# Optimization experiments

Hardware: AMD Instinct MI355X
Metric: run time of the kernel (lower is better)

Reference implementation:

```python
import jax, jax.numpy as jnp
import numpy as np

B, TE, TD, HE, HD = 16, 512, 64, 512, 512


def setup_inputs() -> dict:
    key = jax.random.key(0)
    k1, k2, k3, k4, k5 = jax.random.split(key, 5)
    return {
        "encoder_out_seq": jax.random.normal(k1, (B, TE, HE), dtype=jnp.float32),
        "decoder_out_seq": jax.random.normal(k2, (B, TD, HD), dtype=jnp.float32),
        "W_a": jax.random.normal(k3, (HE, HE), dtype=jnp.float32) * 0.05,
        "U_a": jax.random.normal(k4, (HD, HE), dtype=jnp.float32) * 0.05,
        "V_a": jax.random.normal(k5, (HE, 1), dtype=jnp.float32) * 0.05,
    }


def reference(encoder_out_seq, decoder_out_seq, W_a, U_a, V_a):
    # Bahdanau additive attention, batched over all decoder steps at once
    # (the original K.rnn loop over Td is embarrassingly parallel).
    Ws = jnp.einsum('bte,eh->bth', encoder_out_seq, W_a)   # [B,Te,He]
    Uh = jnp.einsum('bdk,kh->bdh', decoder_out_seq, U_a)   # [B,Td,He]
    # additive combine + tanh: [B,Td,Te,He]
    act = jnp.tanh(Ws[:, None, :, :] + Uh[:, :, None, :])
    e = jnp.einsum('bdth,h->bdt', act, V_a[:, 0])          # [B,Td,Te]
    e = jax.nn.softmax(e, axis=-1)                          # attention weights
    c = jnp.einsum('bdt,bth->bdh', e, encoder_out_seq)      # [B,Td,He] context
    return (c, e)
```

## Files before the change

kernel.cpp:

```cpp
#include <hip/hip_runtime.h>
#include <hip/hip_bf16.h>

#define BB 16
#define TE 512
#define TD 64
#define HE 512

#define PRESCALE 2.8853900817779268f

typedef __attribute__((ext_vector_type(8))) short bf16x8;
typedef __attribute__((ext_vector_type(4))) float f32x4;

__device__ __forceinline__ float fexp2(float x) {
#if __has_builtin(__builtin_amdgcn_exp2f)
    return __builtin_amdgcn_exp2f(x);
#else
    return exp2f(x);
#endif
}
__device__ __forceinline__ float frcp(float x) {
#if __has_builtin(__builtin_amdgcn_rcpf)
    return __builtin_amdgcn_rcpf(x);
#else
    return __fdividef(1.f, x);
#endif
}

__device__ __forceinline__ void split2(float x, unsigned short& h, unsigned short& l) {
    __hip_bfloat16 hb = __float2bfloat16(x);
    h = *(unsigned short*)&hb;
    float r = x - __bfloat162float(hb);
    __hip_bfloat16 lb = __float2bfloat16(r);
    l = *(unsigned short*)&lb;
}

__device__ __forceinline__ void gload16(const unsigned short* g, void* l) {
    __builtin_amdgcn_global_load_lds(
        (const __attribute__((address_space(1))) unsigned int*)g,
        (__attribute__((address_space(3))) unsigned int*)l, 16, 0, 0);
}


__device__ __forceinline__ void tile_load(const float* __restrict__ src, int ld,
                                          float (*tile)[64], int tid)
{
#pragma unroll
    for (int p = 0; p < 4; ++p) {
        const int f = p * 256 + tid;
        const int r = f >> 4, c4 = f & 15;
        const float4 v = *(const float4*)&src[(size_t)r * ld + c4 * 4];
        *(float4*)&tile[r][((c4 ^ (r & 7))) << 2] = v;
    }
}

__device__ __forceinline__ void tile_outA(float (*tile)[64],
                                          unsigned short* __restrict__ H,
                                          unsigned short* __restrict__ L,
                                          size_t Ms, size_t sg_base, size_t m_base, int tid)
{
#pragma unroll
    for (int p = 0; p < 2; ++p) {
        const int task = p * 256 + tid;
        const int s = task >> 6, mm = task & 63;
        const float4 x = *(const float4*)&tile[mm][(((s << 1)    ) ^ (mm & 7)) << 2];
        const float4 y = *(const float4*)&tile[mm][(((s << 1) | 1) ^ (mm & 7)) << 2];
        ushort4 ha, la, hb, lb;
        split2(x.x, ha.x, la.x); split2(x.y, ha.y, la.y);
        split2(x.z, ha.z, la.z); split2(x.w, ha.w, la.w);
        split2(y.x, hb.x, lb.x); split2(y.y, hb.y, lb.y);
        split2(y.z, hb.z, lb.z); split2(y.w, hb.w, lb.w);
        const size_t o = ((sg_base + s) * Ms + m_base + mm) * 8;
        *(ushort4*)&H[o] = ha; *(ushort4*)&H[o + 4] = hb;
        *(ushort4*)&L[o] = la; *(ushort4*)&L[o + 4] = lb;
    }
}

__device__ __forceinline__ void tile_outT(float (*tile)[64],
                                          unsigned short* __restrict__ H,
                                          unsigned short* __restrict__ L,
                                          size_t Ns, size_t sg_base, size_t n_base, int tid)
{
#pragma unroll
    for (int p = 0; p < 2; ++p) {
        const int task = p * 256 + tid;
        const int s2 = task >> 6, hh = task & 63;
        float v[8];
#pragma unroll
        for (int q = 0; q < 8; ++q) {
            const int r = s2 * 8 + q;
            v[q] = tile[r][((((hh >> 2)) ^ (r & 7)) << 2) + (hh & 3)];
        }
        ushort4 ha, la, hb, lb;
        split2(v[0], ha.x, la.x); split2(v[1], ha.y, la.y);
        split2(v[2], ha.z, la.z); split2(v[3], ha.w, la.w);
        split2(v[4], hb.x, lb.x); split2(v[5], hb.y, lb.y);
        split2(v[6], hb.z, lb.z); split2(v[7], hb.w, lb.w);
        const size_t o = ((sg_base + s2) * Ns + n_base + hh) * 8;
        *(ushort4*)&H[o] = ha; *(ushort4*)&H[o + 4] = hb;
        *(ushort4*)&L[o] = la; *(ushort4*)&L[o + 4] = lb;
    }
}

__global__ __launch_bounds__(256)
void split_all(const float* __restrict__ enc,
               unsigned short* __restrict__ eAh, unsigned short* __restrict__ eAl,
               unsigned short* __restrict__ eTh, unsigned short* __restrict__ eTl,
               const float* __restrict__ dec,
               unsigned short* __restrict__ dH, unsigned short* __restrict__ dL,
               const float* __restrict__ Wa,
               unsigned short* __restrict__ wH, unsigned short* __restrict__ wL,
               const float* __restrict__ Ua,
               unsigned short* __restrict__ uH, unsigned short* __restrict__ uL)
{
    __shared__ float tile[64][64];
    const int tid = threadIdx.x;
    const int x = blockIdx.x, y = blockIdx.y, z = blockIdx.z;

    if (z < 16) {
        if (y < 8) {
            const int h0 = x * 64, t0 = y * 64;
            const size_t bo = (size_t)z * TE * HE;
            tile_load(enc + bo + (size_t)t0 * HE + h0, HE, tile, tid);
            __syncthreads();
            tile_outA(tile, eAh, eAl, (size_t)BB * TE, h0 >> 3, (size_t)z * TE + t0, tid);
            tile_outT(tile, eTh + bo, eTl + bo, HE, t0 >> 3, h0, tid);
        } else if (y == 8) {
            const int m0 = z * 64, h0 = x * 64;
            tile_load(dec + (size_t)m0 * HE + h0, HE, tile, tid);
            __syncthreads();
            tile_outA(tile, dH, dL, (size_t)BB * TD, h0 >> 3, m0, tid);
        }
        return;
    }
    const int yy = (y < 8) ? y : y - 8;
    const float* X = (y < 8) ? Wa : Ua;
    unsigned short* H = (y < 8) ? wH : uH;
    unsigned short* L = (y < 8) ? wL : uL;
    const int r0 = yy * 64, c0 = x * 64;
    tile_load(X + (size_t)r0 * HE + c0, HE, tile, tid);
    __syncthreads();
    tile_outT(tile, H, L, HE, r0 >> 3, c0, tid);
}

__global__ __launch_bounds__(256)
void gemm_ws_uh(const unsigned short* __restrict__ eAh, const unsigned short* __restrict__ eAl,
                const unsigned short* __restrict__ wBh, const unsigned short* __restrict__ wBl,
                float* __restrict__ Ew,
                const unsigned short* __restrict__ dAh, const unsigned short* __restrict__ dAl,
                const unsigned short* __restrict__ uBh, const unsigned short* __restrict__ uBl,
                float* __restrict__ Eu)
{
    __shared__ char smem[2][32768];

    const int tid  = threadIdx.x;
    const int lane = tid & 63;
    const int wave = tid >> 6;
    const int wr = wave >> 1, wc = wave & 1;
    const int fr = lane & 15, fg = lane >> 4;

    const int hw = blockIdx.y * 4 + blockIdx.x;
    const int f  = (hw & 7) * 36 + (hw >> 3);
    const int bx = f & 3, by = f >> 2;

    const unsigned short *Ahi, *Alo, *Bhi, *Blo;
    float* C;
    int M, row0;
    if (by < 64) {
        Ahi = eAh; Alo = eAl; Bhi = wBh; Blo = wBl; C = Ew;
        M = BB * TE; row0 = by * 128;
    } else {
        Ahi = dAh; Alo = dAl; Bhi = uBh; Blo = uBl; C = Eu;
        M = BB * TD; row0 = (by - 64) * 128;
    }
    const int N = HE, K = HE;
    const int col0 = bx * 128;

    f32x4 acc[4][4];
#pragma unroll
    for (int mi = 0; mi < 4; ++mi)
#pragma unroll
        for (int ni = 0; ni < 4; ++ni)
            acc[mi][ni] = (f32x4){0.f, 0.f, 0.f, 0.f};

    auto STAGE = [&](int buf, int k0) {
#pragma unroll
        for (int c = 0; c < 2; ++c) {
            const int bi  = (c * 4 + wave) * 64 + lane;
            const int g   = bi >> 7;
            const int idx = bi & 127;
            int mrow = row0 + idx; if (mrow >= M) mrow -= M;
            const int ncol = col0 + idx;
            const size_t ao = ((size_t)((k0 >> 3) + g) * M + mrow) * 8;
            const size_t bo = ((size_t)((k0 >> 3) + g) * N + ncol) * 8;
            const int lb = (c * 4 + wave) * 1024;
            gload16(Ahi + ao, smem[buf] + lb);
            gload16(Alo + ao, smem[buf] + 8192 + lb);
            gload16(Bhi + bo, smem[buf] + 16384 + lb);
            gload16(Blo + bo, smem[buf] + 24576 + lb);
        }
    };

    STAGE(0, 0);

    int buf = 0;
    for (int k0 = 0; k0 < K; k0 += 32) {
        if (k0 + 32 < K) {
            STAGE(buf ^ 1, k0 + 32);
            asm volatile("s_waitcnt vmcnt(8)\n\ts_barrier" ::: "memory");
        } else {
            asm volatile("s_waitcnt vmcnt(0)\n\ts_barrier" ::: "memory");
        }

        const int gb = fg << 7;
        bf16x8 ah[4], al[4], bh[4], bl[4];
#pragma unroll
        for (int mi = 0; mi < 4; ++mi) {
            const int off = (gb + wr * 64 + mi * 16 + fr) * 16;
            ah[mi] = *(const bf16x8*)(smem[buf] + off);
            al[mi] = *(const bf16x8*)(smem[buf] + 8192 + off);
        }
#pragma unroll
        for (int ni = 0; ni < 4; ++ni) {
            const int off = (gb + wc * 64 + ni * 16 + fr) * 16;
            bh[ni] = *(const bf16x8*)(smem[buf] + 16384 + off);
            bl[ni] = *(const bf16x8*)(smem[buf] + 24576 + off);
        }
#pragma unroll
        for (int mi = 0; mi < 4; ++mi)
#pragma unroll
            for (int ni = 0; ni < 4; ++ni) {
                acc[mi][ni] = __builtin_amdgcn_mfma_f32_16x16x32_bf16(ah[mi], bh[ni], acc[mi][ni], 0, 0, 0);
                acc[mi][ni] = __builtin_amdgcn_mfma_f32_16x16x32_bf16(ah[mi], bl[ni], acc[mi][ni], 0, 0, 0);
                acc[mi][ni] = __builtin_amdgcn_mfma_f32_16x16x32_bf16(al[mi], bh[ni], acc[mi][ni], 0, 0, 0);
            }
        asm volatile("s_barrier" ::: "memory");
        buf ^= 1;
    }

#pragma unroll
    for (int mi = 0; mi < 4; ++mi) {
        const int rbase = row0 + wr * 64 + mi * 16 + fg * 4;
#pragma unroll
        for (int ni = 0; ni < 4; ++ni) {
            const int col = col0 + wc * 64 + ni * 16 + fr;
#pragma unroll
            for (int r = 0; r < 4; ++r) {
                const int row = rbase + r;
                if (row < M) C[(size_t)row * N + col] = fexp2(acc[mi][ni][r] * PRESCALE);
            }
        }
    }
}

__global__ __launch_bounds__(256)
void gemm_mfma3(const unsigned short* __restrict__ Ahi, const unsigned short* __restrict__ Alo,
                const unsigned short* __restrict__ Bhi, const unsigned short* __restrict__ Blo,
                float* __restrict__ C, int M, int N, int K,
                long long sA, long long sB, long long sC)
{
    __shared__ char smem[2][32768];

    const int tid  = threadIdx.x;
    const int lane = tid & 63;
    const int wave = tid >> 6;
    const int wr = wave >> 1, wc = wave & 1;
    const int fr = lane & 15, fg = lane >> 4;
    const int row0 = blockIdx.y * 128;
    const int col0 = blockIdx.x * 128;

    Ahi += (size_t)blockIdx.z * sA; Alo += (size_t)blockIdx.z * sA;
    Bhi += (size_t)blockIdx.z * sB; Blo += (size_t)blockIdx.z * sB;
    C   += (size_t)blockIdx.z * sC;

    f32x4 acc[4][4];
#pragma unroll
    for (int mi = 0; mi < 4; ++mi)
#pragma unroll
        for (int ni = 0; ni < 4; ++ni)
            acc[mi][ni] = (f32x4){0.f, 0.f, 0.f, 0.f};

    auto STAGE = [&](int buf, int k0) {
#pragma unroll
        for (int c = 0; c < 2; ++c) {
            const int bi  = (c * 4 + wave) * 64 + lane;
            const int g   = bi >> 7;
            const int idx = bi & 127;
            int mrow = row0 + idx; if (mrow >= M) mrow -= M;
            const int ncol = col0 + idx;
            const size_t ao = ((size_t)((k0 >> 3) + g) * M + mrow) * 8;
            const size_t bo = ((size_t)((k0 >> 3) + g) * N + ncol) * 8;
            const int lb = (c * 4 + wave) * 1024;
            gload16(Ahi + ao, smem[buf] + lb);
            gload16(Alo + ao, smem[buf] + 8192 + lb);
            gload16(Bhi + bo, smem[buf] + 16384 + lb);
            gload16(Blo + bo, smem[buf] + 24576 + lb);
        }
    };

    STAGE(0, 0);

    int buf = 0;
    for (int k0 = 0; k0 < K; k0 += 32) {
        if (k0 + 32 < K) {
            STAGE(buf ^ 1, k0 + 32);
            asm volatile("s_waitcnt vmcnt(8)\n\ts_barrier" ::: "memory");
        } else {
            asm volatile("s_waitcnt vmcnt(0)\n\ts_barrier" ::: "memory");
        }

        const int gb = fg << 7;
        bf16x8 ah[4], al[4], bh[4], bl[4];
#pragma unroll
        for (int mi = 0; mi < 4; ++mi) {
            const int off = (gb + wr * 64 + mi * 16 + fr) * 16;
            ah[mi] = *(const bf16x8*)(smem[buf] + off);
            al[mi] = *(const bf16x8*)(smem[buf] + 8192 + off);
        }
#pragma unroll
        for (int ni = 0; ni < 4; ++ni) {
            const int off = (gb + wc * 64 + ni * 16 + fr) * 16;
            bh[ni] = *(const bf16x8*)(smem[buf] + 16384 + off);
            bl[ni] = *(const bf16x8*)(smem[buf] + 24576 + off);
        }
#pragma unroll
        for (int mi = 0; mi < 4; ++mi)
#pragma unroll
            for (int ni = 0; ni < 4; ++ni) {
                acc[mi][ni] = __builtin_amdgcn_mfma_f32_16x16x32_bf16(ah[mi], bh[ni], acc[mi][ni], 0, 0, 0);
                acc[mi][ni] = __builtin_amdgcn_mfma_f32_16x16x32_bf16(ah[mi], bl[ni], acc[mi][ni], 0, 0, 0);
                acc[mi][ni] = __builtin_amdgcn_mfma_f32_16x16x32_bf16(al[mi], bh[ni], acc[mi][ni], 0, 0, 0);
            }
        asm volatile("s_barrier" ::: "memory");
        buf ^= 1;
    }

#pragma unroll
    for (int mi = 0; mi < 4; ++mi) {
        const int rbase = row0 + wr * 64 + mi * 16 + fg * 4;
#pragma unroll
        for (int ni = 0; ni < 4; ++ni) {
            const int col = col0 + wc * 64 + ni * 16 + fr;
#pragma unroll
            for (int r = 0; r < 4; ++r) {
                const int row = rbase + r;
                if (row < M) C[(size_t)row * N + col] = acc[mi][ni][r];
            }
        }
    }
}

__global__ __launch_bounds__(256)
void gemm_f32(const float* __restrict__ A, const float* __restrict__ Bm,
              float* __restrict__ C, int M, int N, int K,
              long long sAb, long long sBb, long long sCb, float scale, int emode)
{
    __shared__ float As[16][68];
    __shared__ float Bs[16][68];
    const int tid = threadIdx.x;
    const int tx = tid & 15, ty = tid >> 4;
    const int row0 = blockIdx.y * 64, col0 = blockIdx.x * 64;
    A += (long long)blockIdx.z * sAb; Bm += (long long)blockIdx.z * sBb;
    C += (long long)blockIdx.z * sCb;
    float acc[4][4] = {};
    for (int k0 = 0; k0 < K; k0 += 16) {
        {
            const int r = tid >> 2, c = (tid & 3) * 4;
            const float4 av = *(const float4*)&A[(long long)(row0 + r) * K + k0 + c];
            As[c + 0][r] = av.x; As[c + 1][r] = av.y;
            As[c + 2][r] = av.z; As[c + 3][r] = av.w;
        }
        {
            const int r = tid >> 4, c = (tid & 15) * 4;
            *(float4*)&Bs[r][c] = *(const float4*)&Bm[(long long)(k0 + r) * N + col0 + c];
        }
        __syncthreads();
#pragma unroll
        for (int kk = 0; kk < 16; ++kk) {
            const float4 a = *(const float4*)&As[kk][ty * 4];
            const float4 b = *(const float4*)&Bs[kk][tx * 4];
            acc[0][0] += a.x * b.x; acc[0][1] += a.x * b.y; acc[0][2] += a.x * b.z; acc[0][3] += a.x * b.w;
            acc[1][0] += a.y * b.x; acc[1][1] += a.y * b.y; acc[1][2] += a.y * b.z; acc[1][3] += a.y * b.w;
            acc[2][0] += a.z * b.x; acc[2][1] += a.z * b.y; acc[2][2] += a.z * b.z; acc[2][3] += a.z * b.w;
            acc[3][0] += a.w * b.x; acc[3][1] += a.w * b.y; acc[3][2] += a.w * b.z; acc[3][3] += a.w * b.w;
        }
        __syncthreads();
    }
#pragma unroll
    for (int i = 0; i < 4; ++i) {
        float4 o;
        o.x = acc[i][0] * scale; o.y = acc[i][1] * scale;
        o.z = acc[i][2] * scale; o.w = acc[i][3] * scale;
        if (emode) { o.x = fexp2(o.x); o.y = fexp2(o.y); o.z = fexp2(o.z); o.w = fexp2(o.w); }
        *(float4*)&C[(long long)(row0 + ty * 4 + i) * N + col0 + tx * 4] = o;
    }
}

__global__ __launch_bounds__(256)
void scores_raw(const float* __restrict__ Ew, const float* __restrict__ Eu,
                const float* __restrict__ V, float* __restrict__ part)
{
    __shared__ float Ws_s[32][64];
    __shared__ float Uh_s[32][64];
    __shared__ float Vr_s[HE];

    const int tid = threadIdx.x;
    const int tg  = tid & 7;
    const int dg  = tid >> 3;

    const int hw = (blockIdx.z * 8 + blockIdx.y) * 16 + blockIdx.x;
    const int w_ = (hw & 7) * 256 + (hw >> 3);
    const int yy = w_ & 7;
    const int zx = w_ >> 3;
    const int tt0  = (zx & 15) * 32;
    const int quar = yy & 3;
    const int d0   = (yy >> 2) * 32;
    const int b    = zx >> 4;

    const float* Wsg = Ew + (long long)b * TE * HE;
    const float* Uhg = Eu + ((long long)b * TD + d0) * HE;

    if (tid < 128) {
        const float4 v = *(const float4*)&V[tid * 4];
        float4 o; o.x = -2.f * v.x; o.y = -2.f * v.y; o.z = -2.f * v.z; o.w = -2.f * v.w;
        *(float4*)&Vr_s[tid * 4] = o;
    }

    float acc[4] = {0.f, 0.f, 0.f, 0.f};
    const int wswz = tg & 7;
    const int uswz = dg & 7;
    const int hbase = quar * (HE / 4);

    for (int hc = hbase; hc < hbase + HE / 4; hc += 64) {
        __syncthreads();
#pragma unroll
        for (int k = 0; k < 2; ++k) {
            const int idx = tid + k * 256;
            const int r   = idx >> 4;
            const int c4  = idx & 15;
            const float4 wv = *(const float4*)&Wsg[(long long)(tt0 + r) * HE + hc + c4 * 4];
            *(float4*)&Ws_s[r][(c4 ^ ((r >> 2) & 7)) * 4] = wv;
            const float4 uv = *(const float4*)&Uhg[(long long)r * HE + hc + c4 * 4];
            *(float4*)&Uh_s[r][(c4 ^ (r & 7)) * 4] = uv;
        }
        __syncthreads();

#pragma unroll 4
        for (int hs = 0; hs < 64; hs += 4) {
            const int h4 = hs >> 2;
            const float4 vv = *(const float4*)&Vr_s[hc + hs];
            const float4 u  = *(const float4*)&Uh_s[dg][(h4 ^ uswz) * 4];
#pragma unroll
            for (int i = 0; i < 4; ++i) {
                const float4 w = *(const float4*)&Ws_s[tg * 4 + i][(h4 ^ wswz) * 4];
                acc[i] = fmaf(vv.x, frcp(fmaf(w.x, u.x, 1.f)), acc[i]);
                acc[i] = fmaf(vv.y, frcp(fmaf(w.y, u.y, 1.f)), acc[i]);
                acc[i] = fmaf(vv.z, frcp(fmaf(w.z, u.z, 1.f)), acc[i]);
                acc[i] = fmaf(vv.w, frcp(fmaf(w.w, u.w, 1.f)), acc[i]);
            }
        }
    }

    float* dst = part + (size_t)quar * (BB * TD * TE);
    float4 o; o.x = acc[0]; o.y = acc[1]; o.z = acc[2]; o.w = acc[3];
    *(float4*)&dst[((long long)b * TD + d0 + dg) * TE + tt0 + tg * 4] = o;
}

__global__ __launch_bounds__(256)
void softmax_rows(const float* __restrict__ part, float* __restrict__ e,
                  unsigned short* __restrict__ H, unsigned short* __restrict__ L)
{
    const int lane = threadIdx.x & 63;
    const int wave = threadIdx.x >> 6;
    const long long row = blockIdx.x * 4 + wave;

    float4 a = {0.f, 0.f, 0.f, 0.f}, c = {0.f, 0.f, 0.f, 0.f};
#pragma unroll
    for (int q = 0; q < 4; ++q) {
        const float* p = part + (size_t)q * (BB * TD * TE) + row * TE;
        const float4 aq = *(const float4*)&p[lane * 4];
        const float4 cq = *(const float4*)&p[lane * 4 + 256];
        a.x += aq.x; a.y += aq.y; a.z += aq.z; a.w += aq.w;
        c.x += cq.x; c.y += cq.y; c.z += cq.z; c.w += cq.w;
    }

    float m = fmaxf(fmaxf(fmaxf(a.x, a.y), fmaxf(a.z, a.w)),
                    fmaxf(fmaxf(c.x, c.y), fmaxf(c.z, c.w)));
#pragma unroll
    for (int off = 32; off; off >>= 1) m = fmaxf(m, __shfl_xor(m, off));

    a.x = __expf(a.x - m); a.y = __expf(a.y - m); a.z = __expf(a.z - m); a.w = __expf(a.w - m);
    c.x = __expf(c.x - m); c.y = __expf(c.y - m); c.z = __expf(c.z - m); c.w = __expf(c.w - m);

    float s = (a.x + a.y + a.z + a.w) + (c.x + c.y + c.z + c.w);
#pragma unroll
    for (int off = 32; off; off >>= 1) s += __shfl_xor(s, off);

    const float inv = __fdividef(1.f, s);
    a.x *= inv; a.y *= inv; a.z *= inv; a.w *= inv;
    c.x *= inv; c.y *= inv; c.z *= inv; c.w *= inv;
    float* pe = e + row * TE;
    *(float4*)&pe[lane * 4] = a;
    *(float4*)&pe[lane * 4 + 256] = c;

    if (H) {
        const int b = (int)(row >> 6);
        const int d = (int)(row & 63);
        const size_t base = (size_t)b * (TD * TE);
        ushort4 h, l;
        {
            const int t0 = lane * 4;
            const size_t o = base + ((size_t)(t0 >> 3) * TD + d) * 8 + (t0 & 7);
            split2(a.x, h.x, l.x); split2(a.y, h.y, l.y);
            split2(a.z, h.z, l.z); split2(a.w, h.w, l.w);
            *(ushort4*)&H[o] = h;
            *(ushort4*)&L[o] = l;
        }
        {
            const int t0 = lane * 4 + 256;
            const size_t o = base + ((size_t)(t0 >> 3) * TD + d) * 8 + (t0 & 7);
            split2(c.x, h.x, l.x); split2(c.y, h.y, l.y);
            split2(c.z, h.z, l.z); split2(c.w, h.w, l.w);
            *(ushort4*)&H[o] = h;
            *(ushort4*)&L[o] = l;
        }
    }
}

extern "C" void kernel_launch(void* const* d_in, const int* in_sizes, int n_in,
                              void* d_out, int out_size, void* d_ws, size_t ws_size,
                              hipStream_t stream)
{
    const float* enc = (const float*)d_in[0];
    const float* dec = (const float*)d_in[1];
    const float* Wa  = (const float*)d_in[2];
    const float* Ua  = (const float*)d_in[3];
    const float* Va  = (const float*)d_in[4];

    float* out   = (float*)d_out;
    float* c_out = out;
    float* e_out = out + (size_t)BB * TD * HE;

    char* w = (char*)d_ws;
    float* Ew  = (float*)(w);
    float* Eu  = (float*)(w + 16777216);
    unsigned short* encAh = (unsigned short*)(w + 18874368);
    unsigned short* encAl = (unsigned short*)(w + 27262976);
    unsigned short* encTh = (unsigned short*)(w + 35651584);
    unsigned short* encTl = (unsigned short*)(w + 44040192);
    unsigned short* decAh = (unsigned short*)(w + 52428800);
    unsigned short* decAl = (unsigned short*)(w + 53477376);
    unsigned short* WaTh  = (unsigned short*)(w + 54525952);
    unsigned short* WaTl  = (unsigned short*)(w + 55050240);
    unsigned short* UaTh  = (unsigned short*)(w + 55574528);
    unsigned short* UaTl  = (unsigned short*)(w + 56098816);
    unsigned short* eh    = (unsigned short*)(w + 56623104);
    unsigned short* el    = (unsigned short*)(w + 57671680);
    float* part = (float*)(w + 58720256);
    const size_t REQUIRED = 67108864;

    dim3 blk(256);

    if (ws_size >= REQUIRED) {
        split_all<<<dim3(8, 16, 17), blk, 0, stream>>>(
            enc, encAh, encAl, encTh, encTl,
            dec, decAh, decAl, Wa, WaTh, WaTl, Ua, UaTh, UaTl);

        gemm_ws_uh<<<dim3(4, 72, 1), blk, 0, stream>>>(
            encAh, encAl, WaTh, WaTl, Ew, decAh, decAl, UaTh, UaTl, Eu);

        scores_raw<<<dim3(TE / 32, (TD / 32) * 4, BB), blk, 0, stream>>>(Ew, Eu, Va, part);
        softmax_rows<<<dim3(BB * TD / 4), blk, 0, stream>>>(part, e_out, eh, el);

        gemm_mfma3<<<dim3(4, 1, BB), blk, 0, stream>>>(
            eh, el, encTh, encTl, c_out, TD, HE, TE,
            (long long)TD * TE, (long long)TE * HE, (long long)TD * HE);
    } else {
        float* pf = (float*)(w + 18874368);
        gemm_f32<<<dim3(HE / 64, (BB * TE) / 64, 1), blk, 0, stream>>>(
            enc, Wa, Ew, BB * TE, HE, HE, 0, 0, 0, PRESCALE, 1);
        gemm_f32<<<dim3(HE / 64, (BB * TD) / 64, 1), blk, 0, stream>>>(
            dec, Ua, Eu, BB * TD, HE, HE, 0, 0, 0, PRESCALE, 1);
        scores_raw<<<dim3(TE / 32, (TD / 32) * 4, BB), blk, 0, stream>>>(Ew, Eu, Va, pf);
        softmax_rows<<<dim3(BB * TD / 4), blk, 0, stream>>>(pf, e_out, nullptr, nullptr);
        gemm_f32<<<dim3(HE / 64, TD / 64, BB), blk, 0, stream>>>(
            e_out, enc, c_out, TD, HE, TE,
            (long long)TD * TE, (long long)TE * HE, (long long)TD * HE, 1.0f, 0);
    }
}
```

Before: 87.36 us.

## Prefetch second chunk in scores kernel and remap GEMM blocks for L2 locality

The scores kernel now issues global loads for the second 64-wide h chunk into registers before computing on the first chunk, overlapping memory latency with the tanh-sum math. It shrinks the V scratch to only this block's quarter and adds an occupancy hint of 8 blocks per CU. The MFMA GEMM remaps its x/z block indices with an XCD-aware swizzle so that neighbouring tiles share L2. The costs are extra registers held for prefetched data under a tighter register budget, and a remap that assumes the block count divides evenly by 8.

```diff
diff --git a/kernel.cpp b/kernel.cpp
--- a/kernel.cpp
+++ b/kernel.cpp
@@ -253,9 +253,9 @@
 }
 
 __global__ __launch_bounds__(256)
-void gemm_mfma3(const unsigned short* __restrict__ Ahi, const unsigned short* __restrict__ Alo,
-                const unsigned short* __restrict__ Bhi, const unsigned short* __restrict__ Blo,
-                float* __restrict__ C, int M, int N, int K,
+void gemm_mfma3(const unsigned short* __restrict__ Ahi_, const unsigned short* __restrict__ Alo_,
+                const unsigned short* __restrict__ Bhi_, const unsigned short* __restrict__ Blo_,
+                float* __restrict__ C_, int M, int N, int K,
                 long long sA, long long sB, long long sC)
 {
     __shared__ char smem[2][32768];
@@ -265,12 +265,21 @@
     const int wave = tid >> 6;
     const int wr = wave >> 1, wc = wave & 1;
     const int fr = lane & 15, fg = lane >> 4;
+
+    const int nx  = gridDim.x;
+    const int nwg = nx * gridDim.z;
+    const int hw  = blockIdx.z * nx + blockIdx.x;
+    const int w_  = (hw & 7) * (nwg >> 3) + (hw >> 3);
+    const int bz  = w_ / nx, bx = w_ % nx;
+
     const int row0 = blockIdx.y * 128;
-    const int col0 = blockIdx.x * 128;
-
-    Ahi += (size_t)blockIdx.z * sA; Alo += (size_t)blockIdx.z * sA;
-    Bhi += (size_t)blockIdx.z * sB; Blo += (size_t)blockIdx.z * sB;
-    C   += (size_t)blockIdx.z * sC;
+    const int col0 = bx * 128;
+
+    const unsigned short* Ahi = Ahi_ + (size_t)bz * sA;
+    const unsigned short* Alo = Alo_ + (size_t)bz * sA;
+    const unsigned short* Bhi = Bhi_ + (size_t)bz * sB;
+    const unsigned short* Blo = Blo_ + (size_t)bz * sB;
+    float* C = C_ + (size_t)bz * sC;
 
     f32x4 acc[4][4];
 #pragma unroll
@@ -395,13 +404,13 @@
     }
 }
 
-__global__ __launch_bounds__(256)
+__global__ __launch_bounds__(256, 8)
 void scores_raw(const float* __restrict__ Ew, const float* __restrict__ Eu,
                 const float* __restrict__ V, float* __restrict__ part)
 {
     __shared__ float Ws_s[32][64];
     __shared__ float Uh_s[32][64];
-    __shared__ float Vr_s[HE];
+    __shared__ float Vr_s[128];
 
     const int tid = threadIdx.x;
     const int tg  = tid & 7;
@@ -418,45 +427,81 @@
 
     const float* Wsg = Ew + (long long)b * TE * HE;
     const float* Uhg = Eu + ((long long)b * TD + d0) * HE;
-
-    if (tid < 128) {
-        const float4 v = *(const float4*)&V[tid * 4];
+    const int hbase = quar * (HE / 4);
+
+    if (tid < 32) {
+        const float4 v = *(const float4*)&V[hbase + tid * 4];
         float4 o; o.x = -2.f * v.x; o.y = -2.f * v.y; o.z = -2.f * v.z; o.w = -2.f * v.w;
         *(float4*)&Vr_s[tid * 4] = o;
+    }
+
+    int srow[2], scol[2];
+#pragma unroll
+    for (int k = 0; k < 2; ++k) {
+        const int idx = tid + k * 256;
+        srow[k] = idx >> 4;
+        scol[k] = idx & 15;
+    }
+
+    float4 wv[2], uv[2];
+#pragma unroll
+    for (int k = 0; k < 2; ++k) {
+        wv[k] = *(const float4*)&Wsg[(long long)(tt0 + srow[k]) * HE + hbase + scol[k] * 4];
+        uv[k] = *(const float4*)&Uhg[(long long)srow[k] * HE + hbase + scol[k] * 4];
+    }
+#pragma unroll
+    for (int k = 0; k < 2; ++k) {
+        *(float4*)&Ws_s[srow[k]][(scol[k] ^ ((srow[k] >> 2) & 7)) * 4] = wv[k];
+        *(float4*)&Uh_s[srow[k]][(scol[k] ^ (srow[k] & 7)) * 4] = uv[k];
+    }
+    __syncthreads();
+
+    float4 wv1[2], uv1[2];
+#pragma unroll
+    for (int k = 0; k < 2; ++k) {
+        wv1[k] = *(const float4*)&Wsg[(long long)(tt0 + srow[k]) * HE + hbase + 64 + scol[k] * 4];
+        uv1[k] = *(const float4*)&Uhg[(long long)srow[k] * HE + hbase + 64 + scol[k] * 4];
     }
 
     float acc[4] = {0.f, 0.f, 0.f, 0.f};
     const int wswz = tg & 7;
     const int uswz = dg & 7;
-    const int hbase = quar * (HE / 4);
-
-    for (int hc = hbase; hc < hbase + HE / 4; hc += 64) {
-        __syncthreads();
-#pragma unroll
-        for (int k = 0; k < 2; ++k) {
-            const int idx = tid + k * 256;
-            const int r   = idx >> 4;
-            const int c4  = idx & 15;
-            const float4 wv = *(const float4*)&Wsg[(long long)(tt0 + r) * HE + hc + c4 * 4];
-            *(float4*)&Ws_s[r][(c4 ^ ((r >> 2) & 7)) * 4] = wv;
-            const float4 uv = *(const float4*)&Uhg[(long long)r * HE + hc + c4 * 4];
-            *(float4*)&Uh_s[r][(c4 ^ (r & 7)) * 4] = uv;
-        }
-        __syncthreads();
 
 #pragma unroll 4
-        for (int hs = 0; hs < 64; hs += 4) {
-            const int h4 = hs >> 2;
-            const float4 vv = *(const float4*)&Vr_s[hc + hs];
-            const float4 u  = *(const float4*)&Uh_s[dg][(h4 ^ uswz) * 4];
-#pragma unroll
-            for (int i = 0; i < 4; ++i) {
-                const float4 w = *(const float4*)&Ws_s[tg * 4 + i][(h4 ^ wswz) * 4];
-                acc[i] = fmaf(vv.x, frcp(fmaf(w.x, u.x, 1.f)), acc[i]);
-                acc[i] = fmaf(vv.y, frcp(fmaf(w.y, u.y, 1.f)), acc[i]);
-                acc[i] = fmaf(vv.z, frcp(fmaf(w.z, u.z, 1.f)), acc[i]);
-                acc[i] = fmaf(vv.w, frcp(fmaf(w.w, u.w, 1.f)), acc[i]);
-            }
+    for (int hs = 0; hs < 64; hs += 4) {
+        const int h4 = hs >> 2;
+        const float4 vvv = *(const float4*)&Vr_s[hs];
+        const float4 u  = *(const float4*)&Uh_s[dg][(h4 ^ uswz) * 4];
+#pragma unroll
+        for (int i = 0; i < 4; ++i) {
+            const float4 w = *(const float4*)&Ws_s[tg * 4 + i][(h4 ^ wswz) * 4];
+            acc[i] = fmaf(vvv.x, frcp(fmaf(w.x, u.x, 1.f)), acc[i]);
+            acc[i] = fmaf(vvv.y, frcp(fmaf(w.y, u.y, 1.f)), acc[i]);
+            acc[i] = fmaf(vvv.z, frcp(fmaf(w.z, u.z, 1.f)), acc[i]);
+            acc[i] = fmaf(vvv.w, frcp(fmaf(w.w, u.w, 1.f)), acc[i]);
+        }
+    }
+
+    __syncthreads();
+#pragma unroll
+    for (int k = 0; k < 2; ++k) {
+        *(float4*)&Ws_s[srow[k]][(scol[k] ^ ((srow[k] >> 2) & 7)) * 4] = wv1[k];
+        *(float4*)&Uh_s[srow[k]][(scol[k] ^ (srow[k] & 7)) * 4] = uv1[k];
+    }
+    __syncthreads();
+
+#pragma unroll 4
+    for (int hs = 0; hs < 64; hs += 4) {
+        const int h4 = hs >> 2;
+        const float4 vvv = *(const float4*)&Vr_s[64 + hs];
+        const float4 u  = *(const float4*)&Uh_s[dg][(h4 ^ uswz) * 4];
+#pragma unroll
+        for (int i = 0; i < 4; ++i) {
+            const float4 w = *(const float4*)&Ws_s[tg * 4 + i][(h4 ^ wswz) * 4];
+            acc[i] = fmaf(vvv.x, frcp(fmaf(w.x, u.x, 1.f)), acc[i]);
+            acc[i] = fmaf(vvv.y, frcp(fmaf(w.y, u.y, 1.f)), acc[i]);
+            acc[i] = fmaf(vvv.z, frcp(fmaf(w.z, u.z, 1.f)), acc[i]);
+            acc[i] = fmaf(vvv.w, frcp(fmaf(w.w, u.w, 1.f)), acc[i]);
         }
     }
 
```

Measured after the change: 93.45 us. 1.07x slower.
